# Optimization experiments

Hardware: AMD Instinct MI355X
Metric: run time of the kernel (lower is better)

The kernel has to match this reference:

```python
import jax, jax.numpy as jnp
import numpy as np

B, S, D = 16, 2048, 768
NORM = 1.0 / float(np.sqrt(D))


def setup_inputs() -> dict:
    key = jax.random.key(0)
    k1, k2, k3, k4, k5 = jax.random.split(key, 5)
    b_in = jax.random.normal(k1, (B, S, D), dtype=jnp.float32)
    mask = jax.random.randint(k2, (B, S), 0, 2, dtype=jnp.int64)
    # row 0 must be unmasked: the module returns attention[:, 0, :], and a fully
    # masked query row softmaxes all -inf -> NaN (same quirk as the torch source).
    mask = mask.at[:, 0].set(1)
    Wq = jax.random.normal(k3, (D, D), dtype=jnp.float32) * 0.02
    Wk = jax.random.normal(k4, (D, D), dtype=jnp.float32) * 0.02
    Wv = jax.random.normal(k5, (D, D), dtype=jnp.float32) * 0.02
    return {"b_in": b_in, "mask": mask, "Wq": Wq, "Wk": Wk, "Wv": Wv}


def reference(b_in, mask, Wq, Wk, Wv):
    # nn.Linear(bias=False): y = x @ W.T  (W is [out, in])
    q = jnp.einsum("bsd,ed->bse", b_in, Wq)
    k = jnp.einsum("bsd,ed->bse", b_in, Wk)
    v = jnp.einsum("bsd,ed->bse", b_in, Wv)
    # full [B, S, S] score matrix, as in the original bmm
    scores = jnp.einsum("bqd,bkd->bqk", q, k) * NORM
    # mask.unsqueeze(2): [B, S, 1] broadcasts over the KEY axis -> masks whole query rows
    scores = jnp.where(mask[:, :, None] == 0, -jnp.inf, scores)
    attn = jax.nn.softmax(scores, axis=-1)
    out = jnp.einsum("bqk,bkd->bqd", attn, v)
    return out[:, 0, :]
```

## Files before the change

kernel.cpp:

```cpp
#include <hip/hip_runtime.h>
#include <math.h>

#define BB 16
#define SS 2048
#define DD 768

#define NORM_SCALE 0.036084391824351615f

#define ECH 24
#define EPC (DD / ECH)

#define RPC 16
#define NCH (SS / RPC)

__global__ void rowdot_kernel(const float* __restrict__ src, size_t src_stride,
                              const float* __restrict__ W,
                              float* __restrict__ dst, float scale,
                              float* __restrict__ zero_buf) {
    int wid  = blockIdx.x * 4 + (threadIdx.x >> 6);
    int lane = threadIdx.x & 63;
    int b = wid / DD;
    int e = wid % DD;
    const float4* xr = (const float4*)(src + (size_t)b * src_stride);
    const float4* wr = (const float4*)(W + (size_t)e * DD);
    float acc = 0.f;
#pragma unroll
    for (int k = 0; k < 3; ++k) {
        float4 xv = xr[lane + k * 64];
        float4 wv = wr[lane + k * 64];
        acc += xv.x * wv.x + xv.y * wv.y + xv.z * wv.z + xv.w * wv.w;
    }
#pragma unroll
    for (int off = 32; off > 0; off >>= 1) acc += __shfl_down(acc, off);
    if (lane == 0) dst[wid] = acc * scale;
    if (zero_buf != nullptr && lane == 1) zero_buf[wid] = 0.f;
}

__global__ void kq_split_kernel(const float* __restrict__ q0,
                                const float* __restrict__ Wk,
                                float* __restrict__ kqs) {
    __shared__ float qs[EPC];
    int echunk = blockIdx.x;
    int b      = blockIdx.y;
    int t      = threadIdx.x;
    if (t < EPC) qs[t] = q0[b * DD + echunk * EPC + t];
    __syncthreads();
    const float4* Wk4 = (const float4*)(Wk + (size_t)(echunk * EPC) * DD);
    float4 acc = {0.f, 0.f, 0.f, 0.f};
#pragma unroll 4
    for (int e = 0; e < EPC; ++e) {
        float q = qs[e];
        float4 w = Wk4[e * (DD / 4) + t];
        acc.x += q * w.x;
        acc.y += q * w.y;
        acc.z += q * w.z;
        acc.w += q * w.w;
    }
    float* dst = kqs + b * DD + t * 4;
    atomicAdd(dst + 0, acc.x);
    atomicAdd(dst + 1, acc.y);
    atomicAdd(dst + 2, acc.z);
    atomicAdd(dst + 3, acc.w);
}

__global__ void __launch_bounds__(256) flash_kernel(
        const float* __restrict__ x,
        const float* __restrict__ kqs,
        float* __restrict__ m_part,
        float* __restrict__ l_part,
        float* __restrict__ o_part) {
    __shared__ float4 osh[4 * 192];
    __shared__ float sc[RPC];
    __shared__ float wsum[4];
    int chunk = blockIdx.x;
    int b     = blockIdx.y;
    int tid   = threadIdx.x;
    int wave  = tid >> 6, lane = tid & 63;
    int s0    = chunk * RPC;

    const float4* xr = (const float4*)(x + ((size_t)b * SS + s0 + wave * 4) * DD);
    float4 xv[12];
#pragma unroll
    for (int j = 0; j < 4; ++j)
#pragma unroll
        for (int k = 0; k < 3; ++k)
            xv[j * 3 + k] = xr[j * (DD / 4) + k * 64 + lane];

    const float4* kr = (const float4*)(kqs + b * DD);
    float4 kf[3];
#pragma unroll
    for (int k = 0; k < 3; ++k) kf[k] = kr[k * 64 + lane];

#pragma unroll
    for (int j = 0; j < 4; ++j) {
        float acc = 0.f;
#pragma unroll
        for (int k = 0; k < 3; ++k) {
            float4 xx = xv[j * 3 + k];
            acc += xx.x * kf[k].x + xx.y * kf[k].y
                 + xx.z * kf[k].z + xx.w * kf[k].w;
        }
#pragma unroll
        for (int off = 32; off > 0; off >>= 1) acc += __shfl_down(acc, off);
        if (lane == 0) sc[wave * 4 + j] = acc;
    }
    __syncthreads();

    float m = sc[0];
#pragma unroll
    for (int r = 1; r < RPC; ++r) m = fmaxf(m, sc[r]);

    float pl = (lane < 4) ? expf(sc[wave * 4 + lane] - m) : 0.f;
    float p0 = __shfl(pl, 0), p1 = __shfl(pl, 1);
    float p2 = __shfl(pl, 2), p3 = __shfl(pl, 3);
    if (lane == 0) wsum[wave] = p0 + p1 + p2 + p3;

#pragma unroll
    for (int k = 0; k < 3; ++k) {
        float4 a;
        a.x = p0 * xv[k].x + p1 * xv[3 + k].x + p2 * xv[6 + k].x + p3 * xv[9 + k].x;
        a.y = p0 * xv[k].y + p1 * xv[3 + k].y + p2 * xv[6 + k].y + p3 * xv[9 + k].y;
        a.z = p0 * xv[k].z + p1 * xv[3 + k].z + p2 * xv[6 + k].z + p3 * xv[9 + k].z;
        a.w = p0 * xv[k].w + p1 * xv[3 + k].w + p2 * xv[6 + k].w + p3 * xv[9 + k].w;
        osh[wave * 192 + k * 64 + lane] = a;
    }
    __syncthreads();

    int pidx = b * NCH + chunk;
    if (tid < 192) {
        float4 s0v = osh[tid], s1 = osh[192 + tid];
        float4 s2 = osh[384 + tid], s3 = osh[576 + tid];
        float4 s;
        s.x = s0v.x + s1.x + s2.x + s3.x;
        s.y = s0v.y + s1.y + s2.y + s3.y;
        s.z = s0v.z + s1.z + s2.z + s3.z;
        s.w = s0v.w + s1.w + s2.w + s3.w;
        ((float4*)(o_part + (size_t)pidx * DD))[tid] = s;
    }
    if (tid == 0) {
        m_part[pidx] = m;
        l_part[pidx] = wsum[0] + wsum[1] + wsum[2] + wsum[3];
    }
}

__global__ void combine_kernel(const float* __restrict__ m_part,
                               const float* __restrict__ l_part,
                               const float* __restrict__ o_part,
                               float* __restrict__ c) {
    __shared__ float w[NCH];
    __shared__ float bc[2];
    int b   = blockIdx.x;
    int seg = blockIdx.y;
    int tid = threadIdx.x;

    if (tid < 64) {
        float m = fmaxf(m_part[b * NCH + tid], m_part[b * NCH + tid + 64]);
#pragma unroll
        for (int off = 32; off > 0; off >>= 1) m = fmaxf(m, __shfl_down(m, off));
        if (tid == 0) bc[0] = m;
    }
    __syncthreads();
    float M = bc[0];
    if (tid < NCH) w[tid] = expf(m_part[b * NCH + tid] - M);
    __syncthreads();
    if (tid < 64) {
        float s = w[tid] * l_part[b * NCH + tid]
                + w[tid + 64] * l_part[b * NCH + tid + 64];
#pragma unroll
        for (int off = 32; off > 0; off >>= 1) s += __shfl_down(s, off);
        if (tid == 0) bc[1] = 1.f / s;
    }
    __syncthreads();
    float inv = bc[1];

    int col = seg * 256 + tid;
    const float* op = o_part + (size_t)b * NCH * DD + col;
    float a = 0.f;
#pragma unroll 8
    for (int cc = 0; cc < NCH; ++cc) a += w[cc] * op[(size_t)cc * DD];
    c[b * DD + col] = a * inv;
}

extern "C" void kernel_launch(void* const* d_in, const int* in_sizes, int n_in,
                              void* d_out, int out_size, void* d_ws, size_t ws_size,
                              hipStream_t stream) {
    const float* b_in = (const float*)d_in[0];
    const float* Wq = (const float*)d_in[2];
    const float* Wk = (const float*)d_in[3];
    const float* Wv = (const float*)d_in[4];
    float* out = (float*)d_out;

    float* ws     = (float*)d_ws;
    float* q0     = ws;
    float* kqs    = q0 + BB * DD;
    float* m_part = kqs + BB * DD;
    float* l_part = m_part + BB * NCH;
    float* o_part = l_part + BB * NCH;
    float* c      = o_part + (size_t)BB * NCH * DD;

    rowdot_kernel<<<BB * DD / 4, 256, 0, stream>>>(b_in, (size_t)SS * DD, Wq,
                                                   q0, NORM_SCALE, kqs);
    kq_split_kernel<<<dim3(ECH, BB), 192, 0, stream>>>(q0, Wk, kqs);
    flash_kernel<<<dim3(NCH, BB), 256, 0, stream>>>(b_in, kqs,
                                                    m_part, l_part, o_part);
    combine_kernel<<<dim3(BB, 3), 256, 0, stream>>>(m_part, l_part, o_part, c);
    rowdot_kernel<<<BB * DD / 4, 256, 0, stream>>>(c, (size_t)DD, Wv, out,
                                                   1.f, nullptr);
}
```

Baseline: 182.2 us.

## Fuse q projection into prep, drop max-subtraction, accumulate softmax numerator atomically

Result: slower. 191.2 us (+4.9%).

```diff
diff --git a/kernel.cpp b/kernel.cpp
--- a/kernel.cpp
+++ b/kernel.cpp
@@ -13,72 +13,72 @@
 #define RPC 16
 #define NCH (SS / RPC)
 
-__global__ void rowdot_kernel(const float* __restrict__ src, size_t src_stride,
-                              const float* __restrict__ W,
-                              float* __restrict__ dst, float scale,
-                              float* __restrict__ zero_buf) {
-    int wid  = blockIdx.x * 4 + (threadIdx.x >> 6);
-    int lane = threadIdx.x & 63;
-    int b = wid / DD;
-    int e = wid % DD;
-    const float4* xr = (const float4*)(src + (size_t)b * src_stride);
-    const float4* wr = (const float4*)(W + (size_t)e * DD);
-    float acc = 0.f;
-#pragma unroll
-    for (int k = 0; k < 3; ++k) {
-        float4 xv = xr[lane + k * 64];
-        float4 wv = wr[lane + k * 64];
-        acc += xv.x * wv.x + xv.y * wv.y + xv.z * wv.z + xv.w * wv.w;
-    }
-#pragma unroll
-    for (int off = 32; off > 0; off >>= 1) acc += __shfl_down(acc, off);
-    if (lane == 0) dst[wid] = acc * scale;
-    if (zero_buf != nullptr && lane == 1) zero_buf[wid] = 0.f;
-}
-
-__global__ void kq_split_kernel(const float* __restrict__ q0,
-                                const float* __restrict__ Wk,
-                                float* __restrict__ kqs) {
+__global__ void prep_kernel(const float* __restrict__ x,
+                            const float* __restrict__ Wq,
+                            const float* __restrict__ Wk,
+                            float* __restrict__ kqs) {
     __shared__ float qs[EPC];
     int echunk = blockIdx.x;
     int b      = blockIdx.y;
-    int t      = threadIdx.x;
-    if (t < EPC) qs[t] = q0[b * DD + echunk * EPC + t];
+    int tid    = threadIdx.x;
+    int wave   = tid >> 6, lane = tid & 63;
+
+    const float4* xr = (const float4*)(x + (size_t)b * SS * DD);
+    float4 xf[3];
+#pragma unroll
+    for (int k = 0; k < 3; ++k) xf[k] = xr[k * 64 + lane];
+
+#pragma unroll
+    for (int j = 0; j < 8; ++j) {
+        int el = wave * 8 + j;
+        const float4* wr = (const float4*)(Wq + (size_t)(echunk * EPC + el) * DD);
+        float acc = 0.f;
+#pragma unroll
+        for (int k = 0; k < 3; ++k) {
+            float4 wv = wr[k * 64 + lane];
+            acc += xf[k].x * wv.x + xf[k].y * wv.y
+                 + xf[k].z * wv.z + xf[k].w * wv.w;
+        }
+#pragma unroll
+        for (int off = 32; off > 0; off >>= 1) acc += __shfl_down(acc, off);
+        if (lane == 0) qs[el] = acc * NORM_SCALE;
+    }
     __syncthreads();
-    const float4* Wk4 = (const float4*)(Wk + (size_t)(echunk * EPC) * DD);
-    float4 acc = {0.f, 0.f, 0.f, 0.f};
+
+    if (tid < 192) {
+        const float4* Wk4 = (const float4*)(Wk + (size_t)(echunk * EPC) * DD);
+        float4 acc = {0.f, 0.f, 0.f, 0.f};
 #pragma unroll 4
-    for (int e = 0; e < EPC; ++e) {
-        float q = qs[e];
-        float4 w = Wk4[e * (DD / 4) + t];
-        acc.x += q * w.x;
-        acc.y += q * w.y;
-        acc.z += q * w.z;
-        acc.w += q * w.w;
+        for (int e = 0; e < EPC; ++e) {
+            float q = qs[e];
+            float4 w = Wk4[e * (DD / 4) + tid];
+            acc.x += q * w.x;
+            acc.y += q * w.y;
+            acc.z += q * w.z;
+            acc.w += q * w.w;
+        }
+        float* dst = kqs + b * DD + tid * 4;
+        atomicAdd(dst + 0, acc.x);
+        atomicAdd(dst + 1, acc.y);
+        atomicAdd(dst + 2, acc.z);
+        atomicAdd(dst + 3, acc.w);
     }
-    float* dst = kqs + b * DD + t * 4;
-    atomicAdd(dst + 0, acc.x);
-    atomicAdd(dst + 1, acc.y);
-    atomicAdd(dst + 2, acc.z);
-    atomicAdd(dst + 3, acc.w);
 }
 
 __global__ void __launch_bounds__(256) flash_kernel(
         const float* __restrict__ x,
         const float* __restrict__ kqs,
-        float* __restrict__ m_part,
-        float* __restrict__ l_part,
-        float* __restrict__ o_part) {
+        float* __restrict__ l,
+        float* __restrict__ c_num) {
     __shared__ float4 osh[4 * 192];
-    __shared__ float sc[RPC];
     __shared__ float wsum[4];
     int chunk = blockIdx.x;
     int b     = blockIdx.y;
     int tid   = threadIdx.x;
     int wave  = tid >> 6, lane = tid & 63;
-    int s0    = chunk * RPC;
 
-    const float4* xr = (const float4*)(x + ((size_t)b * SS + s0 + wave * 4) * DD);
+    const float4* xr =
+        (const float4*)(x + ((size_t)b * SS + chunk * RPC + wave * 4) * DD);
     float4 xv[12];
 #pragma unroll
     for (int j = 0; j < 4; ++j)
@@ -91,6 +91,7 @@
 #pragma unroll
     for (int k = 0; k < 3; ++k) kf[k] = kr[k * 64 + lane];
 
+    float p[4];
 #pragma unroll
     for (int j = 0; j < 4; ++j) {
         float acc = 0.f;
@@ -102,83 +103,53 @@
         }
 #pragma unroll
         for (int off = 32; off > 0; off >>= 1) acc += __shfl_down(acc, off);
-        if (lane == 0) sc[wave * 4 + j] = acc;
+        p[j] = expf(__shfl(acc, 0));
     }
-    __syncthreads();
-
-    float m = sc[0];
-#pragma unroll
-    for (int r = 1; r < RPC; ++r) m = fmaxf(m, sc[r]);
-
-    float pl = (lane < 4) ? expf(sc[wave * 4 + lane] - m) : 0.f;
-    float p0 = __shfl(pl, 0), p1 = __shfl(pl, 1);
-    float p2 = __shfl(pl, 2), p3 = __shfl(pl, 3);
-    if (lane == 0) wsum[wave] = p0 + p1 + p2 + p3;
+    if (lane == 0) wsum[wave] = p[0] + p[1] + p[2] + p[3];
 
 #pragma unroll
     for (int k = 0; k < 3; ++k) {
         float4 a;
-        a.x = p0 * xv[k].x + p1 * xv[3 + k].x + p2 * xv[6 + k].x + p3 * xv[9 + k].x;
-        a.y = p0 * xv[k].y + p1 * xv[3 + k].y + p2 * xv[6 + k].y + p3 * xv[9 + k].y;
-        a.z = p0 * xv[k].z + p1 * xv[3 + k].z + p2 * xv[6 + k].z + p3 * xv[9 + k].z;
-        a.w = p0 * xv[k].w + p1 * xv[3 + k].w + p2 * xv[6 + k].w + p3 * xv[9 + k].w;
+        a.x = p[0] * xv[k].x + p[1] * xv[3 + k].x + p[2] * xv[6 + k].x + p[3] * xv[9 + k].x;
+        a.y = p[0] * xv[k].y + p[1] * xv[3 + k].y + p[2] * xv[6 + k].y + p[3] * xv[9 + k].y;
+        a.z = p[0] * xv[k].z + p[1] * xv[3 + k].z + p[2] * xv[6 + k].z + p[3] * xv[9 + k].z;
+        a.w = p[0] * xv[k].w + p[1] * xv[3 + k].w + p[2] * xv[6 + k].w + p[3] * xv[9 + k].w;
         osh[wave * 192 + k * 64 + lane] = a;
     }
     __syncthreads();
 
-    int pidx = b * NCH + chunk;
+    if (tid == 0) atomicAdd(&l[b], wsum[0] + wsum[1] + wsum[2] + wsum[3]);
     if (tid < 192) {
-        float4 s0v = osh[tid], s1 = osh[192 + tid];
+        float4 s0 = osh[tid], s1 = osh[192 + tid];
         float4 s2 = osh[384 + tid], s3 = osh[576 + tid];
-        float4 s;
-        s.x = s0v.x + s1.x + s2.x + s3.x;
-        s.y = s0v.y + s1.y + s2.y + s3.y;
-        s.z = s0v.z + s1.z + s2.z + s3.z;
-        s.w = s0v.w + s1.w + s2.w + s3.w;
-        ((float4*)(o_part + (size_t)pidx * DD))[tid] = s;
-    }
-    if (tid == 0) {
-        m_part[pidx] = m;
-        l_part[pidx] = wsum[0] + wsum[1] + wsum[2] + wsum[3];
+        float* dst = c_num + b * DD + tid * 4;
+        atomicAdd(dst + 0, s0.x + s1.x + s2.x + s3.x);
+        atomicAdd(dst + 1, s0.y + s1.y + s2.y + s3.y);
+        atomicAdd(dst + 2, s0.z + s1.z + s2.z + s3.z);
+        atomicAdd(dst + 3, s0.w + s1.w + s2.w + s3.w);
     }
 }
 
-__global__ void combine_kernel(const float* __restrict__ m_part,
-                               const float* __restrict__ l_part,
-                               const float* __restrict__ o_part,
-                               float* __restrict__ c) {
-    __shared__ float w[NCH];
-    __shared__ float bc[2];
-    int b   = blockIdx.x;
-    int seg = blockIdx.y;
-    int tid = threadIdx.x;
-
-    if (tid < 64) {
-        float m = fmaxf(m_part[b * NCH + tid], m_part[b * NCH + tid + 64]);
+__global__ void out_kernel(const float* __restrict__ c_num,
+                           const float* __restrict__ l,
+                           const float* __restrict__ Wv,
+                           float* __restrict__ out) {
+    int wid  = blockIdx.x * 4 + (threadIdx.x >> 6);
+    int lane = threadIdx.x & 63;
+    int b = wid / DD;
+    int e = wid % DD;
+    const float4* cr = (const float4*)(c_num + (size_t)b * DD);
+    const float4* wr = (const float4*)(Wv + (size_t)e * DD);
+    float acc = 0.f;
 #pragma unroll
-        for (int off = 32; off > 0; off >>= 1) m = fmaxf(m, __shfl_down(m, off));
-        if (tid == 0) bc[0] = m;
+    for (int k = 0; k < 3; ++k) {
+        float4 cv = cr[lane + k * 64];
+        float4 wv = wr[lane + k * 64];
+        acc += cv.x * wv.x + cv.y * wv.y + cv.z * wv.z + cv.w * wv.w;
     }
-    __syncthreads();
-    float M = bc[0];
-    if (tid < NCH) w[tid] = expf(m_part[b * NCH + tid] - M);
-    __syncthreads();
-    if (tid < 64) {
-        float s = w[tid] * l_part[b * NCH + tid]
-                + w[tid + 64] * l_part[b * NCH + tid + 64];
 #pragma unroll
-        for (int off = 32; off > 0; off >>= 1) s += __shfl_down(s, off);
-        if (tid == 0) bc[1] = 1.f / s;
-    }
-    __syncthreads();
-    float inv = bc[1];
-
-    int col = seg * 256 + tid;
-    const float* op = o_part + (size_t)b * NCH * DD + col;
-    float a = 0.f;
-#pragma unroll 8
-    for (int cc = 0; cc < NCH; ++cc) a += w[cc] * op[(size_t)cc * DD];
-    c[b * DD + col] = a * inv;
+    for (int off = 32; off > 0; off >>= 1) acc += __shfl_down(acc, off);
+    if (lane == 0) out[wid] = acc / l[b];
 }
 
 extern "C" void kernel_launch(void* const* d_in, const int* in_sizes, int n_in,
@@ -190,20 +161,14 @@
     const float* Wv = (const float*)d_in[4];
     float* out = (float*)d_out;
 
-    float* ws     = (float*)d_ws;
-    float* q0     = ws;
-    float* kqs    = q0 + BB * DD;
-    float* m_part = kqs + BB * DD;
-    float* l_part = m_part + BB * NCH;
-    float* o_part = l_part + BB * NCH;
-    float* c      = o_part + (size_t)BB * NCH * DD;
+    float* ws    = (float*)d_ws;
+    float* kqs   = ws;
+    float* c_num = kqs + BB * DD;
+    float* l     = c_num + BB * DD;
+    size_t zero_bytes = (size_t)(2 * BB * DD + BB) * sizeof(float);
 
-    rowdot_kernel<<<BB * DD / 4, 256, 0, stream>>>(b_in, (size_t)SS * DD, Wq,
-                                                   q0, NORM_SCALE, kqs);
-    kq_split_kernel<<<dim3(ECH, BB), 192, 0, stream>>>(q0, Wk, kqs);
-    flash_kernel<<<dim3(NCH, BB), 256, 0, stream>>>(b_in, kqs,
-                                                    m_part, l_part, o_part);
-    combine_kernel<<<dim3(BB, 3), 256, 0, stream>>>(m_part, l_part, o_part, c);
-    rowdot_kernel<<<BB * DD / 4, 256, 0, stream>>>(c, (size_t)DD, Wv, out,
-                                                   1.f, nullptr);
+    hipMemsetAsync(ws, 0, zero_bytes, stream);
+    prep_kernel<<<dim3(ECH, BB), 256, 0, stream>>>(b_in, Wq, Wk, kqs);
+    flash_kernel<<<dim3(NCH, BB), 256, 0, stream>>>(b_in, kqs, l, c_num);
+    out_kernel<<<BB * DD / 4, 256, 0, stream>>>(c_num, l, Wv, out);
 }
```
